# Kernel optimization log

Hardware: AMD Instinct MI355X
Metric: run time of the kernel (lower is better)

## Reference

```python
import jax, jax.numpy as jnp
import numpy as np

TEMPERATURE = 0.1


def setup_inputs() -> dict:
    key = jax.random.key(0)
    k1, k2 = jax.random.split(key)
    B, B_pos, D = 8192, 8192, 1024
    generated = jax.random.normal(k1, (B, D), dtype=jnp.float32)
    positive = jax.random.normal(k2, (B_pos, D), dtype=jnp.float32)
    return {"generated": generated, "positive": positive}


def _pairwise_dist_sq(x, y):
    # (N, M) squared L2 distances, clamped at 0
    x_norm = jnp.sum(x * x, axis=-1, keepdims=True)          # (N, 1)
    y_norm = jnp.sum(y * y, axis=-1, keepdims=True)          # (M, 1)
    d2 = x_norm + y_norm.T - 2.0 * (x @ y.T)
    return jnp.clip(d2, 0.0)


def reference(generated, positive):
    gen = generated.reshape(generated.shape[0], -1)
    pos = positive.reshape(positive.shape[0], -1)
    B = gen.shape[0]

    # Attraction: softmax over distances to positives.
    dist_pos = jnp.sqrt(_pairwise_dist_sq(gen, pos))          # (B, B_pos)
    w_pos = jax.nn.softmax(-dist_pos / TEMPERATURE, axis=1)
    # sum_j w_ij (pos_j - gen_i) == (w_pos @ pos) - gen  (rows of w sum to 1)
    attraction = w_pos @ pos - gen                            # (B, D)

    # Repulsion: softmax over distances to other generated samples (diag masked).
    d2_neg = _pairwise_dist_sq(gen, gen)
    eye = jnp.eye(B, dtype=bool)
    dist_neg = jnp.sqrt(jnp.where(eye, jnp.inf, d2_neg))      # inf diag -> weight 0
    w_neg = jax.nn.softmax(-dist_neg / TEMPERATURE, axis=1)
    repulsion = w_neg @ gen - gen                             # (B, D)

    drift = attraction - repulsion
    target = jax.lax.stop_gradient(gen + drift)
    loss = jnp.mean((gen - target) ** 2)

    drift_norm = jnp.mean(jnp.linalg.norm(drift, axis=-1))
    attraction_norm = jnp.mean(jnp.linalg.norm(attraction, axis=-1))
    repulsion_norm = jnp.mean(jnp.linalg.norm(repulsion, axis=-1))
    return (loss, drift_norm, attraction_norm, repulsion_norm)
```

## Files before the change

kernel.cpp:

```cpp
#include <hip/hip_runtime.h>
#include <stdint.h>

#define INV_T 10.0f
#define SHIFT_ 460.0f
#define MROWS 8192
#define DDIM 1024
#define CHUNK 1024

typedef __attribute__((ext_vector_type(8))) short bf16x8;
typedef __attribute__((ext_vector_type(4))) float f32x4;

__device__ __forceinline__ float bf2f(unsigned short u) {
  return __uint_as_float(((unsigned int)u) << 16);
}
__device__ __forceinline__ unsigned short f2bf(float f) {
  unsigned int u = __float_as_uint(f);
  return (unsigned short)((u + 0x7FFFu + ((u >> 16) & 1u)) >> 16);
}
__device__ __forceinline__ void gl2lds16(const unsigned short* g, unsigned short* l) {
  __builtin_amdgcn_global_load_lds((const __attribute__((address_space(1))) void*)g,
                                   (__attribute__((address_space(3))) void*)l, 16, 0, 0);
}

__global__ void prep_kernel(const float* __restrict__ gen, const float* __restrict__ pos,
                            unsigned short* __restrict__ gen_h, unsigned short* __restrict__ pos_h,
                            float* __restrict__ gn2, float* __restrict__ pn2) {
  int b = blockIdx.x;
  const float* src; unsigned short* dst; float* n2; int row;
  if (b < MROWS) { src = gen; dst = gen_h; n2 = gn2; row = b; }
  else           { src = pos; dst = pos_h; n2 = pn2; row = b - MROWS; }
  int t = threadIdx.x;
  float4 v = ((const float4*)(src + (size_t)row * DDIM))[t];
  float ss = v.x * v.x + v.y * v.y + v.z * v.z + v.w * v.w;
  ushort4 o;
  o.x = f2bf(v.x); o.y = f2bf(v.y); o.z = f2bf(v.z); o.w = f2bf(v.w);
  ((ushort4*)(dst + (size_t)row * DDIM))[t] = o;
#pragma unroll
  for (int m = 1; m < 64; m <<= 1) ss += __shfl_xor(ss, m);
  __shared__ float red[4];
  if ((t & 63) == 0) red[t >> 6] = ss;
  __syncthreads();
  if (t == 0) n2[row] = red[0] + red[1] + red[2] + red[3];
}

__global__ void transpose_kernel(const float* __restrict__ gen, const float* __restrict__ pos,
                                 unsigned short* __restrict__ genT, unsigned short* __restrict__ posT) {
  __shared__ float tile[64][65];
  int b = blockIdx.x;
  const float* src; unsigned short* dst;
  if (b < 2048) { src = gen; dst = genT; }
  else          { src = pos; dst = posT; b -= 2048; }
  int tj = b >> 4, td = b & 15;
  int t = threadIdx.x;
#pragma unroll
  for (int it = 0; it < 16; ++it) {
    int idx = it * 256 + t;
    int r = idx >> 6, c = idx & 63;
    tile[r][c] = src[(size_t)(tj * 64 + r) * DDIM + td * 64 + c];
  }
  __syncthreads();
#pragma unroll
  for (int it = 0; it < 16; ++it) {
    int idx = it * 256 + t;
    int d = idx >> 6, j = idx & 63;
    dst[(size_t)(td * 64 + d) * MROWS + tj * 64 + j] = f2bf(tile[j][d]);
  }
}

template <int EPI>
__launch_bounds__(256, 2)
__global__ void gemm_bt(const unsigned short* __restrict__ A0, const unsigned short* __restrict__ A1,
                        long lda,
                        const unsigned short* __restrict__ B0, const unsigned short* __restrict__ B1,
                        long ldb, int ksteps,
                        unsigned short* __restrict__ P0, unsigned short* __restrict__ P1,
                        int pld, int j0,
                        const float* __restrict__ qn2,
                        const float* __restrict__ kn2a, const float* __restrict__ kn2b,
                        float* __restrict__ lsum0, float* __restrict__ lsum1,
                        unsigned short* __restrict__ O0, unsigned short* __restrict__ O1,
                        int first) {
  __shared__ __align__(16) unsigned short Al[128 * 64];
  __shared__ __align__(16) unsigned short Bl[128 * 64];
  const int z = blockIdx.z;
  const unsigned short* A = z ? A1 : A0;
  const unsigned short* B = z ? B1 : B0;
  const int t = threadIdx.x;
  const int w = t >> 6, lane = t & 63, l15 = lane & 15, quad = lane >> 4;
  const int wm = w >> 1, wn = w & 1;
  const long m0 = (long)blockIdx.x * 128;
  const long n0 = (long)blockIdx.y * 128;
  const int trow = t >> 3;
  const int tcol = (((t & 7) ^ (trow & 7)) * 8);

  f32x4 acc[4][4];
#pragma unroll
  for (int i = 0; i < 4; ++i)
#pragma unroll
    for (int j = 0; j < 4; ++j) acc[i][j] = (f32x4){0.f, 0.f, 0.f, 0.f};

  const unsigned short* Ab = A + (m0 + trow) * lda + tcol;
  const unsigned short* Bb = B + (n0 + trow) * ldb + tcol;
  unsigned short* Alw = Al + t * 8;
  unsigned short* Blw = Bl + t * 8;
  const int ue = (quad ^ (l15 & 7)) * 8;

  for (int ks = 0; ks < ksteps; ++ks) {
    const long ko = (long)ks * 64;
#pragma unroll
    for (int i = 0; i < 4; ++i) gl2lds16(Ab + (long)i * 32 * lda + ko, Alw + i * 2048);
#pragma unroll
    for (int i = 0; i < 4; ++i) gl2lds16(Bb + (long)i * 32 * ldb + ko, Blw + i * 2048);
    __syncthreads();
#pragma unroll
    for (int kk = 0; kk < 2; ++kk) {
      const int uo = ue ^ (kk * 32);
      bf16x8 af[4], bfr[4];
#pragma unroll
      for (int mi = 0; mi < 4; ++mi)
        af[mi] = *(const bf16x8*)(Al + (wm * 64 + mi * 16 + l15) * 64 + uo);
#pragma unroll
      for (int ni = 0; ni < 4; ++ni)
        bfr[ni] = *(const bf16x8*)(Bl + (wn * 64 + ni * 16 + l15) * 64 + uo);
#pragma unroll
      for (int mi = 0; mi < 4; ++mi)
#pragma unroll
        for (int ni = 0; ni < 4; ++ni)
          acc[mi][ni] = __builtin_amdgcn_mfma_f32_16x16x32_bf16(af[mi], bfr[ni], acc[mi][ni], 0, 0, 0);
    }
    __syncthreads();
  }

  if (EPI == 0) {
    unsigned short* Pout = z ? P1 : P0;
    const float* kn2 = z ? kn2b : kn2a;
    float* lsum = z ? lsum1 : lsum0;
#pragma unroll
    for (int mi = 0; mi < 4; ++mi) {
      float rs[4] = {0.f, 0.f, 0.f, 0.f};
#pragma unroll
      for (int ni = 0; ni < 4; ++ni) {
        int c = (int)n0 + wn * 64 + ni * 16 + l15;
        float kn = kn2[j0 + c];
#pragma unroll
        for (int reg = 0; reg < 4; ++reg) {
          long r = m0 + wm * 64 + mi * 16 + quad * 4 + reg;
          float v = acc[mi][ni][reg];
          float d2 = qn2[r] + kn - 2.0f * v;
          float p = __expf(SHIFT_ - INV_T * sqrtf(fmaxf(d2, 0.0f)));
          if (z && (int)r == (j0 + c)) p = 0.0f;
          rs[reg] += p;
          Pout[r * (long)pld + c] = f2bf(p);
        }
      }
#pragma unroll
      for (int reg = 0; reg < 4; ++reg) {
        float v = rs[reg];
        v += __shfl_xor(v, 1); v += __shfl_xor(v, 2);
        v += __shfl_xor(v, 4); v += __shfl_xor(v, 8);
        if (l15 == 0) atomicAdd(&lsum[m0 + wm * 64 + mi * 16 + quad * 4 + reg], v);
      }
    }
  } else {
    unsigned short* Oh = z ? O1 : O0;
#pragma unroll
    for (int mi = 0; mi < 4; ++mi)
#pragma unroll
      for (int ni = 0; ni < 4; ++ni) {
        long c = n0 + wn * 64 + ni * 16 + l15;
#pragma unroll
        for (int reg = 0; reg < 4; ++reg) {
          long r = m0 + wm * 64 + mi * 16 + quad * 4 + reg;
          long off = r * DDIM + c;
          float v = acc[mi][ni][reg];
          Oh[off] = f2bf(first ? v : (bf2f(Oh[off]) + v));
        }
      }
  }
}

__global__ void epi_kernel(const unsigned short* __restrict__ OA, const unsigned short* __restrict__ OR_,
                           const float* __restrict__ lsumA, const float* __restrict__ lsumR,
                           const float* __restrict__ genf, float* __restrict__ gs) {
  __shared__ float wsL[4], wsD[4], wsA[4], wsR[4];
  const int t = threadIdx.x;
  const int w = t >> 6;
  const int lane = t & 63;
  float accL = 0.f, accD = 0.f, accA = 0.f, accR = 0.f;

  for (int i = 0; i < 8; ++i) {
    const int row = blockIdx.x * 32 + w * 8 + i;
    const float invlA = 1.0f / lsumA[row];
    const float invlR = 1.0f / lsumR[row];
    float ssA = 0.f, ssR = 0.f, ssD = 0.f;
#pragma unroll
    for (int u = 0; u < 4; ++u) {
      const long off = (long)row * DDIM + u * 256 + lane * 4;
      float4 g = *(const float4*)(genf + off);
      ushort4 oa = *(const ushort4*)(OA + off);
      ushort4 orr = *(const ushort4*)(OR_ + off);
      float g4[4] = {g.x, g.y, g.z, g.w};
      float a4[4] = {bf2f(oa.x), bf2f(oa.y), bf2f(oa.z), bf2f(oa.w)};
      float r4[4] = {bf2f(orr.x), bf2f(orr.y), bf2f(orr.z), bf2f(orr.w)};
#pragma unroll
      for (int e = 0; e < 4; ++e) {
        float a_ = a4[e] * invlA - g4[e];
        float r_ = r4[e] * invlR - g4[e];
        float d_ = a_ - r_;
        ssA += a_ * a_; ssR += r_ * r_; ssD += d_ * d_;
      }
    }
#pragma unroll
    for (int m = 1; m < 64; m <<= 1) {
      ssA += __shfl_xor(ssA, m);
      ssR += __shfl_xor(ssR, m);
      ssD += __shfl_xor(ssD, m);
    }
    accA += sqrtf(ssA); accR += sqrtf(ssR); accD += sqrtf(ssD); accL += ssD;
  }
  if (lane == 0) { wsL[w] = accL; wsD[w] = accD; wsA[w] = accA; wsR[w] = accR; }
  __syncthreads();
  if (t == 0) {
    atomicAdd(&gs[0], wsL[0] + wsL[1] + wsL[2] + wsL[3]);
    atomicAdd(&gs[1], wsD[0] + wsD[1] + wsD[2] + wsD[3]);
    atomicAdd(&gs[2], wsA[0] + wsA[1] + wsA[2] + wsA[3]);
    atomicAdd(&gs[3], wsR[0] + wsR[1] + wsR[2] + wsR[3]);
  }
}

__global__ void finalize_kernel(const float* __restrict__ gs, float* __restrict__ out) {
  int t = threadIdx.x;
  if (t == 0) out[0] = gs[0] / (8192.0f * 1024.0f);
  if (t == 1) out[1] = gs[1] / 8192.0f;
  if (t == 2) out[2] = gs[2] / 8192.0f;
  if (t == 3) out[3] = gs[3] / 8192.0f;
}

extern "C" void kernel_launch(void* const* d_in, const int* in_sizes, int n_in,
                              void* d_out, int out_size, void* d_ws, size_t ws_size,
                              hipStream_t stream) {
  const float* gen = (const float*)d_in[0];
  const float* pos = (const float*)d_in[1];
  char* ws = (char*)d_ws;
  const size_t MB = (size_t)1 << 20;
  unsigned short* gen_h = (unsigned short*)(ws + 0 * MB);
  unsigned short* pos_h = (unsigned short*)(ws + 16 * MB);
  unsigned short* genT  = (unsigned short*)(ws + 32 * MB);
  unsigned short* posT  = (unsigned short*)(ws + 48 * MB);
  unsigned short* Pa    = (unsigned short*)(ws + 64 * MB);
  unsigned short* Pr    = (unsigned short*)(ws + 80 * MB);
  unsigned short* OhA   = (unsigned short*)(ws + 96 * MB);
  unsigned short* OhR   = (unsigned short*)(ws + 112 * MB);
  float* gn2   = (float*)(ws + 128 * MB);
  float* pn2   = (float*)(ws + 128 * MB + 32768);
  float* lsumA = (float*)(ws + 128 * MB + 65536);
  float* lsumR = (float*)(ws + 128 * MB + 98304);
  float* gs    = (float*)(ws + 128 * MB + 131072);

  hipMemsetAsync(gs, 0, 4 * sizeof(float), stream);
  hipMemsetAsync(lsumA, 0, 2 * MROWS * sizeof(float), stream);
  prep_kernel<<<dim3(16384), dim3(256), 0, stream>>>(gen, pos, gen_h, pos_h, gn2, pn2);
  transpose_kernel<<<dim3(4096), dim3(256), 0, stream>>>(gen, pos, genT, posT);

  const int nchunks = MROWS / CHUNK;
  for (int c = 0; c < nchunks; ++c) {
    const int j0 = c * CHUNK;
    gemm_bt<0><<<dim3(64, CHUNK / 128, 2), dim3(256), 0, stream>>>(
        gen_h, gen_h, DDIM,
        pos_h + (long)j0 * DDIM, gen_h + (long)j0 * DDIM, DDIM, DDIM / 64,
        Pa, Pr, CHUNK, j0, gn2, pn2, gn2, lsumA, lsumR, nullptr, nullptr, 0);
    gemm_bt<1><<<dim3(64, DDIM / 128, 2), dim3(256), 0, stream>>>(
        Pa, Pr, CHUNK,
        posT + j0, genT + j0, MROWS, CHUNK / 64,
        nullptr, nullptr, 0, 0, nullptr, nullptr, nullptr, nullptr, nullptr,
        OhA, OhR, c == 0);
  }

  epi_kernel<<<dim3(256), dim3(256), 0, stream>>>(OhA, OhR, lsumA, lsumR, gen, gs);
  finalize_kernel<<<dim3(1), dim3(64), 0, stream>>>(gs, (float*)d_out);
}
```

Measured before the change: 905.4 us.

## Use 256x256 tiles with 8 waves and a double-buffered pipelined LDS schedule

Measured after the change: 1.021 ms. 1.13x slower.

```diff
diff --git a/kernel.cpp b/kernel.cpp
--- a/kernel.cpp
+++ b/kernel.cpp
@@ -68,7 +68,7 @@
 }
 
 template <int EPI>
-__launch_bounds__(256, 2)
+__launch_bounds__(512, 2)
 __global__ void gemm_bt(const unsigned short* __restrict__ A0, const unsigned short* __restrict__ A1,
                         long lda,
                         const unsigned short* __restrict__ B0, const unsigned short* __restrict__ B1,
@@ -80,63 +80,158 @@
                         float* __restrict__ lsum0, float* __restrict__ lsum1,
                         unsigned short* __restrict__ O0, unsigned short* __restrict__ O1,
                         int first) {
-  __shared__ __align__(16) unsigned short Al[128 * 64];
-  __shared__ __align__(16) unsigned short Bl[128 * 64];
+  __shared__ __align__(16) unsigned short Asm[2][256 * 64];
+  __shared__ __align__(16) unsigned short Bsm[2][256 * 64];
   const int z = blockIdx.z;
   const unsigned short* A = z ? A1 : A0;
   const unsigned short* B = z ? B1 : B0;
   const int t = threadIdx.x;
-  const int w = t >> 6, lane = t & 63, l15 = lane & 15, quad = lane >> 4;
-  const int wm = w >> 1, wn = w & 1;
-  const long m0 = (long)blockIdx.x * 128;
-  const long n0 = (long)blockIdx.y * 128;
+  const int lane = t & 63, l15 = lane & 15, quad = lane >> 4;
+  const int w = t >> 6, wm = w >> 2, wn = w & 3;
+  const long m0 = (long)blockIdx.x * 256;
+  const long n0 = (long)blockIdx.y * 256;
   const int trow = t >> 3;
-  const int tcol = (((t & 7) ^ (trow & 7)) * 8);
-
-  f32x4 acc[4][4];
-#pragma unroll
-  for (int i = 0; i < 4; ++i)
+  const int tcol = ((t & 7) ^ (trow & 7)) * 8;
+  const int uo = (quad ^ (l15 & 7)) * 8;
+
+  const unsigned short* const Ag = A + (m0 + trow) * lda + tcol;
+  const unsigned short* const Bg = B + (n0 + trow) * ldb + tcol;
+
+  f32x4 acc[8][4];
+#pragma unroll
+  for (int i = 0; i < 8; ++i)
 #pragma unroll
     for (int j = 0; j < 4; ++j) acc[i][j] = (f32x4){0.f, 0.f, 0.f, 0.f};
 
-  const unsigned short* Ab = A + (m0 + trow) * lda + tcol;
-  const unsigned short* Bb = B + (n0 + trow) * ldb + tcol;
-  unsigned short* Alw = Al + t * 8;
-  unsigned short* Blw = Bl + t * 8;
-  const int ue = (quad ^ (l15 & 7)) * 8;
+#define ST_A(dst, ko, hf)                                                 \
+  do {                                                                    \
+    const unsigned short* s_ = Ag + (long)((hf) * 128) * lda + (ko);      \
+    unsigned short* d_ = (dst) + (hf) * 8192 + t * 8;                     \
+    gl2lds16(s_, d_);                                                     \
+    gl2lds16(s_ + 64 * lda, d_ + 4096);                                   \
+  } while (0)
+#define ST_B(dst, ko, hf)                                                 \
+  do {                                                                    \
+    const unsigned short* s_ = Bg + (long)((hf) * 128) * ldb + (ko);      \
+    unsigned short* d_ = (dst) + (hf) * 8192 + t * 8;                     \
+    gl2lds16(s_, d_);                                                     \
+    gl2lds16(s_ + 64 * ldb, d_ + 4096);                                   \
+  } while (0)
+
+  ST_A(Asm[0], 0, 0); ST_A(Asm[0], 0, 1);
+  ST_B(Bsm[0], 0, 0); ST_B(Bsm[0], 0, 1);
+  ST_A(Asm[1], 64, 0);
+  asm volatile("s_waitcnt vmcnt(2)" ::: "memory");
+  __builtin_amdgcn_s_barrier();
+
+  unsigned short* Ac = Asm[0]; unsigned short* An = Asm[1];
+  unsigned short* Bc = Bsm[0]; unsigned short* Bn = Bsm[1];
+  const int rbA = (wm * 128 + l15) * 64;
+  const int rbB = (wn * 64 + l15) * 64;
+
+  bf16x8 aR[4][2], bLo[2][2], bHi[2][2];
 
   for (int ks = 0; ks < ksteps; ++ks) {
-    const long ko = (long)ks * 64;
-#pragma unroll
-    for (int i = 0; i < 4; ++i) gl2lds16(Ab + (long)i * 32 * lda + ko, Alw + i * 2048);
-#pragma unroll
-    for (int i = 0; i < 4; ++i) gl2lds16(Bb + (long)i * 32 * ldb + ko, Blw + i * 2048);
-    __syncthreads();
-#pragma unroll
-    for (int kk = 0; kk < 2; ++kk) {
-      const int uo = ue ^ (kk * 32);
-      bf16x8 af[4], bfr[4];
-#pragma unroll
-      for (int mi = 0; mi < 4; ++mi)
-        af[mi] = *(const bf16x8*)(Al + (wm * 64 + mi * 16 + l15) * 64 + uo);
-#pragma unroll
-      for (int ni = 0; ni < 4; ++ni)
-        bfr[ni] = *(const bf16x8*)(Bl + (wn * 64 + ni * 16 + l15) * 64 + uo);
-#pragma unroll
-      for (int mi = 0; mi < 4; ++mi)
-#pragma unroll
-        for (int ni = 0; ni < 4; ++ni)
-          acc[mi][ni] = __builtin_amdgcn_mfma_f32_16x16x32_bf16(af[mi], bfr[ni], acc[mi][ni], 0, 0, 0);
+    const long ko1 = (long)(ks + 1) * 64;
+    const long ko2 = (long)(ks + 2) * 64;
+    const bool s1 = (ks + 1 < ksteps), s2 = (ks + 2 < ksteps);
+
+#pragma unroll
+    for (int mi = 0; mi < 4; ++mi)
+#pragma unroll
+      for (int kk = 0; kk < 2; ++kk)
+        aR[mi][kk] = *(const bf16x8*)(Ac + rbA + mi * 1024 + (uo ^ (kk * 32)));
+#pragma unroll
+    for (int ni = 0; ni < 2; ++ni)
+#pragma unroll
+      for (int kk = 0; kk < 2; ++kk)
+        bLo[ni][kk] = *(const bf16x8*)(Bc + rbB + ni * 1024 + (uo ^ (kk * 32)));
+    if (s1) ST_A(An, ko1, 1);
+    __builtin_amdgcn_s_barrier();
+    asm volatile("s_waitcnt lgkmcnt(0)" ::: "memory");
+    __builtin_amdgcn_sched_barrier(0);
+    __builtin_amdgcn_s_setprio(1);
+#pragma unroll
+    for (int mi = 0; mi < 4; ++mi)
+#pragma unroll
+      for (int ni = 0; ni < 2; ++ni)
+#pragma unroll
+        for (int kk = 0; kk < 2; ++kk)
+          acc[mi][ni] = __builtin_amdgcn_mfma_f32_16x16x32_bf16(aR[mi][kk], bLo[ni][kk], acc[mi][ni], 0, 0, 0);
+    __builtin_amdgcn_s_setprio(0);
+    __builtin_amdgcn_s_barrier();
+
+#pragma unroll
+    for (int ni = 0; ni < 2; ++ni)
+#pragma unroll
+      for (int kk = 0; kk < 2; ++kk)
+        bHi[ni][kk] = *(const bf16x8*)(Bc + rbB + (ni + 2) * 1024 + (uo ^ (kk * 32)));
+    if (s1) ST_B(Bn, ko1, 0);
+    __builtin_amdgcn_s_barrier();
+    asm volatile("s_waitcnt lgkmcnt(0)" ::: "memory");
+    __builtin_amdgcn_sched_barrier(0);
+    __builtin_amdgcn_s_setprio(1);
+#pragma unroll
+    for (int mi = 0; mi < 4; ++mi)
+#pragma unroll
+      for (int ni = 0; ni < 2; ++ni)
+#pragma unroll
+        for (int kk = 0; kk < 2; ++kk)
+          acc[mi][ni + 2] = __builtin_amdgcn_mfma_f32_16x16x32_bf16(aR[mi][kk], bHi[ni][kk], acc[mi][ni + 2], 0, 0, 0);
+    __builtin_amdgcn_s_setprio(0);
+    __builtin_amdgcn_s_barrier();
+
+#pragma unroll
+    for (int mi = 0; mi < 4; ++mi)
+#pragma unroll
+      for (int kk = 0; kk < 2; ++kk)
+        aR[mi][kk] = *(const bf16x8*)(Ac + rbA + (mi + 4) * 1024 + (uo ^ (kk * 32)));
+    if (s1) ST_B(Bn, ko1, 1);
+    __builtin_amdgcn_s_barrier();
+    asm volatile("s_waitcnt lgkmcnt(0)" ::: "memory");
+    __builtin_amdgcn_sched_barrier(0);
+    __builtin_amdgcn_s_setprio(1);
+#pragma unroll
+    for (int mi = 0; mi < 4; ++mi)
+#pragma unroll
+      for (int ni = 0; ni < 2; ++ni)
+#pragma unroll
+        for (int kk = 0; kk < 2; ++kk)
+          acc[mi + 4][ni + 2] = __builtin_amdgcn_mfma_f32_16x16x32_bf16(aR[mi][kk], bHi[ni][kk], acc[mi + 4][ni + 2], 0, 0, 0);
+    __builtin_amdgcn_s_setprio(0);
+    __builtin_amdgcn_s_barrier();
+
+    if (s2) {
+      ST_A(Ac, ko2, 0);
+      asm volatile("s_waitcnt vmcnt(2)" ::: "memory");
+    } else {
+      asm volatile("s_waitcnt vmcnt(0)" ::: "memory");
     }
-    __syncthreads();
-  }
+    __builtin_amdgcn_s_barrier();
+    __builtin_amdgcn_s_setprio(1);
+#pragma unroll
+    for (int mi = 0; mi < 4; ++mi)
+#pragma unroll
+      for (int ni = 0; ni < 2; ++ni)
+#pragma unroll
+        for (int kk = 0; kk < 2; ++kk)
+          acc[mi + 4][ni] = __builtin_amdgcn_mfma_f32_16x16x32_bf16(aR[mi][kk], bLo[ni][kk], acc[mi + 4][ni], 0, 0, 0);
+    __builtin_amdgcn_s_setprio(0);
+    __builtin_amdgcn_s_barrier();
+
+    unsigned short* tp;
+    tp = Ac; Ac = An; An = tp;
+    tp = Bc; Bc = Bn; Bn = tp;
+  }
+#undef ST_A
+#undef ST_B
 
   if (EPI == 0) {
     unsigned short* Pout = z ? P1 : P0;
     const float* kn2 = z ? kn2b : kn2a;
     float* lsum = z ? lsum1 : lsum0;
 #pragma unroll
-    for (int mi = 0; mi < 4; ++mi) {
+    for (int mi = 0; mi < 8; ++mi) {
       float rs[4] = {0.f, 0.f, 0.f, 0.f};
 #pragma unroll
       for (int ni = 0; ni < 4; ++ni) {
@@ -144,7 +239,7 @@
         float kn = kn2[j0 + c];
 #pragma unroll
         for (int reg = 0; reg < 4; ++reg) {
-          long r = m0 + wm * 64 + mi * 16 + quad * 4 + reg;
+          long r = m0 + wm * 128 + mi * 16 + quad * 4 + reg;
           float v = acc[mi][ni][reg];
           float d2 = qn2[r] + kn - 2.0f * v;
           float p = __expf(SHIFT_ - INV_T * sqrtf(fmaxf(d2, 0.0f)));
@@ -158,19 +253,19 @@
         float v = rs[reg];
         v += __shfl_xor(v, 1); v += __shfl_xor(v, 2);
         v += __shfl_xor(v, 4); v += __shfl_xor(v, 8);
-        if (l15 == 0) atomicAdd(&lsum[m0 + wm * 64 + mi * 16 + quad * 4 + reg], v);
+        if (l15 == 0) atomicAdd(&lsum[m0 + wm * 128 + mi * 16 + quad * 4 + reg], v);
       }
     }
   } else {
     unsigned short* Oh = z ? O1 : O0;
 #pragma unroll
-    for (int mi = 0; mi < 4; ++mi)
+    for (int mi = 0; mi < 8; ++mi)
 #pragma unroll
       for (int ni = 0; ni < 4; ++ni) {
         long c = n0 + wn * 64 + ni * 16 + l15;
 #pragma unroll
         for (int reg = 0; reg < 4; ++reg) {
-          long r = m0 + wm * 64 + mi * 16 + quad * 4 + reg;
+          long r = m0 + wm * 128 + mi * 16 + quad * 4 + reg;
           long off = r * DDIM + c;
           float v = acc[mi][ni][reg];
           Oh[off] = f2bf(first ? v : (bf2f(Oh[off]) + v));
@@ -265,11 +360,11 @@
   const int nchunks = MROWS / CHUNK;
   for (int c = 0; c < nchunks; ++c) {
     const int j0 = c * CHUNK;
-    gemm_bt<0><<<dim3(64, CHUNK / 128, 2), dim3(256), 0, stream>>>(
+    gemm_bt<0><<<dim3(MROWS / 256, CHUNK / 256, 2), dim3(512), 0, stream>>>(
         gen_h, gen_h, DDIM,
         pos_h + (long)j0 * DDIM, gen_h + (long)j0 * DDIM, DDIM, DDIM / 64,
         Pa, Pr, CHUNK, j0, gn2, pn2, gn2, lsumA, lsumR, nullptr, nullptr, 0);
-    gemm_bt<1><<<dim3(64, DDIM / 128, 2), dim3(256), 0, stream>>>(
+    gemm_bt<1><<<dim3(MROWS / 256, DDIM / 256, 2), dim3(512), 0, stream>>>(
         Pa, Pr, CHUNK,
         posT + j0, genT + j0, MROWS, CHUNK / 64,
         nullptr, nullptr, 0, 0, nullptr, nullptr, nullptr, nullptr, nullptr,
```

## Share query tile across attraction/repulsion GEMMs and double-chunk the PV GEMM

Applied to the files above, without the earlier changes.

New measurement: 814.2 us. 10.1% less time.

```diff
diff --git a/kernel.cpp b/kernel.cpp
--- a/kernel.cpp
+++ b/kernel.cpp
@@ -67,29 +67,190 @@
   }
 }
 
-template <int EPI>
 __launch_bounds__(256, 2)
-__global__ void gemm_bt(const unsigned short* __restrict__ A0, const unsigned short* __restrict__ A1,
-                        long lda,
-                        const unsigned short* __restrict__ B0, const unsigned short* __restrict__ B1,
-                        long ldb, int ksteps,
-                        unsigned short* __restrict__ P0, unsigned short* __restrict__ P1,
-                        int pld, int j0,
-                        const float* __restrict__ qn2,
-                        const float* __restrict__ kn2a, const float* __restrict__ kn2b,
-                        float* __restrict__ lsum0, float* __restrict__ lsum1,
-                        unsigned short* __restrict__ O0, unsigned short* __restrict__ O1,
+__global__ void gemm_sc(const unsigned short* __restrict__ Aq,
+                        const unsigned short* __restrict__ Bka,
+                        const unsigned short* __restrict__ Bkr,
+                        unsigned short* __restrict__ Pa, unsigned short* __restrict__ Pr,
+                        int j0,
+                        const float* __restrict__ gn2, const float* __restrict__ pn2,
+                        float* __restrict__ lsumA, float* __restrict__ lsumR) {
+  __shared__ __align__(16) unsigned short Al[128 * 64];
+  __shared__ __align__(16) unsigned short Bal[128 * 64];
+  __shared__ __align__(16) unsigned short Brl[128 * 64];
+
+  const int orig = blockIdx.x + 64 * blockIdx.y;
+  const int wid = (orig & 7) * 64 + (orig >> 3);
+  const int by = wid & 7;
+  const int bx = wid >> 3;
+
+  const int t = threadIdx.x;
+  const int w = t >> 6, lane = t & 63, l15 = lane & 15, quad = lane >> 4;
+  const int wm = w >> 1, wn = w & 1;
+  const long m0 = (long)bx * 128;
+  const long n0 = (long)by * 128;
+  const int trow = t >> 3;
+  const int tcol = (((t & 7) ^ (trow & 7)) * 8);
+
+  f32x4 accA[4][4], accR[4][4];
+#pragma unroll
+  for (int i = 0; i < 4; ++i)
+#pragma unroll
+    for (int j = 0; j < 4; ++j) {
+      accA[i][j] = (f32x4){0.f, 0.f, 0.f, 0.f};
+      accR[i][j] = (f32x4){0.f, 0.f, 0.f, 0.f};
+    }
+
+  const unsigned short* Ab  = Aq  + (m0 + trow) * DDIM + tcol;
+  const unsigned short* Bab = Bka + (n0 + trow) * DDIM + tcol;
+  const unsigned short* Brb = Bkr + (n0 + trow) * DDIM + tcol;
+  unsigned short* Alw = Al  + t * 8;
+  unsigned short* Baw = Bal + t * 8;
+  unsigned short* Brw = Brl + t * 8;
+  const int ue = (quad ^ (l15 & 7)) * 8;
+
+  for (int ks = 0; ks < DDIM / 64; ++ks) {
+    const long ko = (long)ks * 64;
+#pragma unroll
+    for (int i = 0; i < 4; ++i) gl2lds16(Ab + (long)i * 32 * DDIM + ko, Alw + i * 2048);
+#pragma unroll
+    for (int i = 0; i < 4; ++i) gl2lds16(Bab + (long)i * 32 * DDIM + ko, Baw + i * 2048);
+#pragma unroll
+    for (int i = 0; i < 4; ++i) gl2lds16(Brb + (long)i * 32 * DDIM + ko, Brw + i * 2048);
+    __syncthreads();
+#pragma unroll
+    for (int kk = 0; kk < 2; ++kk) {
+      const int uo = ue ^ (kk * 32);
+      bf16x8 af[4], ba[4], br[4];
+#pragma unroll
+      for (int mi = 0; mi < 4; ++mi)
+        af[mi] = *(const bf16x8*)(Al + (wm * 64 + mi * 16 + l15) * 64 + uo);
+#pragma unroll
+      for (int ni = 0; ni < 4; ++ni) {
+        ba[ni] = *(const bf16x8*)(Bal + (wn * 64 + ni * 16 + l15) * 64 + uo);
+        br[ni] = *(const bf16x8*)(Brl + (wn * 64 + ni * 16 + l15) * 64 + uo);
+      }
+#pragma unroll
+      for (int mi = 0; mi < 4; ++mi)
+#pragma unroll
+        for (int ni = 0; ni < 4; ++ni) {
+          accA[mi][ni] = __builtin_amdgcn_mfma_f32_16x16x32_bf16(af[mi], ba[ni], accA[mi][ni], 0, 0, 0);
+          accR[mi][ni] = __builtin_amdgcn_mfma_f32_16x16x32_bf16(af[mi], br[ni], accR[mi][ni], 0, 0, 0);
+        }
+    }
+    __syncthreads();
+  }
+
+#pragma unroll
+  for (int mi = 0; mi < 4; ++mi) {
+    float rs[4] = {0.f, 0.f, 0.f, 0.f};
+#pragma unroll
+    for (int ni = 0; ni < 4; ++ni) {
+      int c = (int)n0 + wn * 64 + ni * 16 + l15;
+      float kn = pn2[j0 + c];
+#pragma unroll
+      for (int reg = 0; reg < 4; ++reg) {
+        long r = m0 + wm * 64 + mi * 16 + quad * 4 + reg;
+        float v = accA[mi][ni][reg];
+        float d2 = gn2[r] + kn - 2.0f * v;
+        float p = __expf(SHIFT_ - INV_T * sqrtf(fmaxf(d2, 0.0f)));
+        rs[reg] += p;
+        Pa[r * (long)CHUNK + c] = f2bf(p);
+      }
+    }
+#pragma unroll
+    for (int reg = 0; reg < 4; ++reg) {
+      float v = rs[reg];
+      v += __shfl_xor(v, 1); v += __shfl_xor(v, 2);
+      v += __shfl_xor(v, 4); v += __shfl_xor(v, 8);
+      if (l15 == 0) atomicAdd(&lsumA[m0 + wm * 64 + mi * 16 + quad * 4 + reg], v);
+    }
+  }
+#pragma unroll
+  for (int mi = 0; mi < 4; ++mi) {
+    float rs[4] = {0.f, 0.f, 0.f, 0.f};
+#pragma unroll
+    for (int ni = 0; ni < 4; ++ni) {
+      int c = (int)n0 + wn * 64 + ni * 16 + l15;
+      float kn = gn2[j0 + c];
+#pragma unroll
+      for (int reg = 0; reg < 4; ++reg) {
+        long r = m0 + wm * 64 + mi * 16 + quad * 4 + reg;
+        float v = accR[mi][ni][reg];
+        float d2 = gn2[r] + kn - 2.0f * v;
+        float p = __expf(SHIFT_ - INV_T * sqrtf(fmaxf(d2, 0.0f)));
+        if ((int)r == (j0 + c)) p = 0.0f;
+        rs[reg] += p;
+        Pr[r * (long)CHUNK + c] = f2bf(p);
+      }
+    }
+#pragma unroll
+    for (int reg = 0; reg < 4; ++reg) {
+      float v = rs[reg];
+      v += __shfl_xor(v, 1); v += __shfl_xor(v, 2);
+      v += __shfl_xor(v, 4); v += __shfl_xor(v, 8);
+      if (l15 == 0) atomicAdd(&lsumR[m0 + wm * 64 + mi * 16 + quad * 4 + reg], v);
+    }
+  }
+}
+
+#define KSEG(Abase, Bbase, LDA_, LDB_)                                                     \
+  {                                                                                        \
+    const unsigned short* Ab_ = (Abase) + (m0 + trow) * (LDA_) + tcol;                     \
+    const unsigned short* Bb_ = (Bbase) + (n0 + trow) * (LDB_) + tcol;                     \
+    for (int ks = 0; ks < 16; ++ks) {                                                      \
+      const long ko = (long)ks * 64;                                                       \
+      _Pragma("unroll")                                                                    \
+      for (int i = 0; i < 4; ++i) gl2lds16(Ab_ + (long)i * 32 * (LDA_) + ko, Alw + i * 2048); \
+      _Pragma("unroll")                                                                    \
+      for (int i = 0; i < 4; ++i) gl2lds16(Bb_ + (long)i * 32 * (LDB_) + ko, Blw + i * 2048); \
+      __syncthreads();                                                                     \
+      _Pragma("unroll")                                                                    \
+      for (int kk = 0; kk < 2; ++kk) {                                                     \
+        const int uo = ue ^ (kk * 32);                                                     \
+        bf16x8 af[4], bfr[4];                                                              \
+        _Pragma("unroll")                                                                  \
+        for (int mi = 0; mi < 4; ++mi)                                                     \
+          af[mi] = *(const bf16x8*)(Al + (wm * 64 + mi * 16 + l15) * 64 + uo);             \
+        _Pragma("unroll")                                                                  \
+        for (int ni = 0; ni < 4; ++ni)                                                     \
+          bfr[ni] = *(const bf16x8*)(Bl + (wn * 64 + ni * 16 + l15) * 64 + uo);            \
+        _Pragma("unroll")                                                                  \
+        for (int mi = 0; mi < 4; ++mi)                                                     \
+          _Pragma("unroll")                                                                \
+          for (int ni = 0; ni < 4; ++ni)                                                   \
+            acc[mi][ni] = __builtin_amdgcn_mfma_f32_16x16x32_bf16(af[mi], bfr[ni], acc[mi][ni], 0, 0, 0); \
+      }                                                                                    \
+      __syncthreads();                                                                     \
+    }                                                                                      \
+  }
+
+__launch_bounds__(256, 2)
+__global__ void gemm_pv(const unsigned short* __restrict__ Pa0, const unsigned short* __restrict__ Pr0,
+                        const unsigned short* __restrict__ Pa1, const unsigned short* __restrict__ Pr1,
+                        const unsigned short* __restrict__ Va0, const unsigned short* __restrict__ Vr0,
+                        const unsigned short* __restrict__ Va1, const unsigned short* __restrict__ Vr1,
+                        unsigned short* __restrict__ OA, unsigned short* __restrict__ OR_,
                         int first) {
   __shared__ __align__(16) unsigned short Al[128 * 64];
   __shared__ __align__(16) unsigned short Bl[128 * 64];
-  const int z = blockIdx.z;
-  const unsigned short* A = z ? A1 : A0;
-  const unsigned short* B = z ? B1 : B0;
+
+  const int orig = blockIdx.x + 64 * (blockIdx.y + 8 * blockIdx.z);
+  const int wid = (orig & 7) * 128 + (orig >> 3);
+  const int by = wid & 7;
+  const int bx = (wid >> 3) & 63;
+  const int z = wid >> 9;
+
+  const unsigned short* A0 = z ? Pr0 : Pa0;
+  const unsigned short* B0 = z ? Vr0 : Va0;
+  const unsigned short* A1 = z ? Pr1 : Pa1;
+  const unsigned short* B1 = z ? Vr1 : Va1;
+
   const int t = threadIdx.x;
   const int w = t >> 6, lane = t & 63, l15 = lane & 15, quad = lane >> 4;
   const int wm = w >> 1, wn = w & 1;
-  const long m0 = (long)blockIdx.x * 128;
-  const long n0 = (long)blockIdx.y * 128;
+  const long m0 = (long)bx * 128;
+  const long n0 = (long)by * 128;
   const int trow = t >> 3;
   const int tcol = (((t & 7) ^ (trow & 7)) * 8);
 
@@ -99,85 +260,29 @@
 #pragma unroll
     for (int j = 0; j < 4; ++j) acc[i][j] = (f32x4){0.f, 0.f, 0.f, 0.f};
 
-  const unsigned short* Ab = A + (m0 + trow) * lda + tcol;
-  const unsigned short* Bb = B + (n0 + trow) * ldb + tcol;
   unsigned short* Alw = Al + t * 8;
   unsigned short* Blw = Bl + t * 8;
   const int ue = (quad ^ (l15 & 7)) * 8;
 
-  for (int ks = 0; ks < ksteps; ++ks) {
-    const long ko = (long)ks * 64;
-#pragma unroll
-    for (int i = 0; i < 4; ++i) gl2lds16(Ab + (long)i * 32 * lda + ko, Alw + i * 2048);
-#pragma unroll
-    for (int i = 0; i < 4; ++i) gl2lds16(Bb + (long)i * 32 * ldb + ko, Blw + i * 2048);
-    __syncthreads();
-#pragma unroll
-    for (int kk = 0; kk < 2; ++kk) {
-      const int uo = ue ^ (kk * 32);
-      bf16x8 af[4], bfr[4];
-#pragma unroll
-      for (int mi = 0; mi < 4; ++mi)
-        af[mi] = *(const bf16x8*)(Al + (wm * 64 + mi * 16 + l15) * 64 + uo);
-#pragma unroll
-      for (int ni = 0; ni < 4; ++ni)
-        bfr[ni] = *(const bf16x8*)(Bl + (wn * 64 + ni * 16 + l15) * 64 + uo);
-#pragma unroll
-      for (int mi = 0; mi < 4; ++mi)
-#pragma unroll
-        for (int ni = 0; ni < 4; ++ni)
-          acc[mi][ni] = __builtin_amdgcn_mfma_f32_16x16x32_bf16(af[mi], bfr[ni], acc[mi][ni], 0, 0, 0);
-    }
-    __syncthreads();
-  }
-
-  if (EPI == 0) {
-    unsigned short* Pout = z ? P1 : P0;
-    const float* kn2 = z ? kn2b : kn2a;
-    float* lsum = z ? lsum1 : lsum0;
-#pragma unroll
-    for (int mi = 0; mi < 4; ++mi) {
-      float rs[4] = {0.f, 0.f, 0.f, 0.f};
-#pragma unroll
-      for (int ni = 0; ni < 4; ++ni) {
-        int c = (int)n0 + wn * 64 + ni * 16 + l15;
-        float kn = kn2[j0 + c];
-#pragma unroll
-        for (int reg = 0; reg < 4; ++reg) {
-          long r = m0 + wm * 64 + mi * 16 + quad * 4 + reg;
-          float v = acc[mi][ni][reg];
-          float d2 = qn2[r] + kn - 2.0f * v;
-          float p = __expf(SHIFT_ - INV_T * sqrtf(fmaxf(d2, 0.0f)));
-          if (z && (int)r == (j0 + c)) p = 0.0f;
-          rs[reg] += p;
-          Pout[r * (long)pld + c] = f2bf(p);
-        }
-      }
+  KSEG(A0, B0, CHUNK, MROWS);
+  KSEG(A1, B1, CHUNK, MROWS);
+
+  unsigned short* Oh = z ? OR_ : OA;
+#pragma unroll
+  for (int mi = 0; mi < 4; ++mi)
+#pragma unroll
+    for (int ni = 0; ni < 4; ++ni) {
+      long c = n0 + wn * 64 + ni * 16 + l15;
 #pragma unroll
       for (int reg = 0; reg < 4; ++reg) {
-        float v = rs[reg];
-        v += __shfl_xor(v, 1); v += __shfl_xor(v, 2);
-        v += __shfl_xor(v, 4); v += __shfl_xor(v, 8);
-        if (l15 == 0) atomicAdd(&lsum[m0 + wm * 64 + mi * 16 + quad * 4 + reg], v);
-      }
-    }
-  } else {
-    unsigned short* Oh = z ? O1 : O0;
-#pragma unroll
-    for (int mi = 0; mi < 4; ++mi)
-#pragma unroll
-      for (int ni = 0; ni < 4; ++ni) {
-        long c = n0 + wn * 64 + ni * 16 + l15;
-#pragma unroll
-        for (int reg = 0; reg < 4; ++reg) {
-          long r = m0 + wm * 64 + mi * 16 + quad * 4 + reg;
-          long off = r * DDIM + c;
-          float v = acc[mi][ni][reg];
-          Oh[off] = f2bf(first ? v : (bf2f(Oh[off]) + v));
-        }
-      }
-  }
-}
+        long r = m0 + wm * 64 + mi * 16 + quad * 4 + reg;
+        long off = r * DDIM + c;
+        float v = acc[mi][ni][reg];
+        Oh[off] = f2bf(first ? v : (bf2f(Oh[off]) + v));
+      }
+    }
+}
+#undef KSEG
 
 __global__ void epi_kernel(const unsigned short* __restrict__ OA, const unsigned short* __restrict__ OR_,
                            const float* __restrict__ lsumA, const float* __restrict__ lsumR,
@@ -247,33 +352,35 @@
   unsigned short* pos_h = (unsigned short*)(ws + 16 * MB);
   unsigned short* genT  = (unsigned short*)(ws + 32 * MB);
   unsigned short* posT  = (unsigned short*)(ws + 48 * MB);
-  unsigned short* Pa    = (unsigned short*)(ws + 64 * MB);
-  unsigned short* Pr    = (unsigned short*)(ws + 80 * MB);
-  unsigned short* OhA   = (unsigned short*)(ws + 96 * MB);
-  unsigned short* OhR   = (unsigned short*)(ws + 112 * MB);
-  float* gn2   = (float*)(ws + 128 * MB);
-  float* pn2   = (float*)(ws + 128 * MB + 32768);
-  float* lsumA = (float*)(ws + 128 * MB + 65536);
-  float* lsumR = (float*)(ws + 128 * MB + 98304);
-  float* gs    = (float*)(ws + 128 * MB + 131072);
+  unsigned short* Pa0   = (unsigned short*)(ws + 64 * MB);
+  unsigned short* Pr0   = (unsigned short*)(ws + 80 * MB);
+  unsigned short* Pa1   = (unsigned short*)(ws + 96 * MB);
+  unsigned short* Pr1   = (unsigned short*)(ws + 112 * MB);
+  unsigned short* OhA   = (unsigned short*)(ws + 128 * MB);
+  unsigned short* OhR   = (unsigned short*)(ws + 144 * MB);
+  float* gn2   = (float*)(ws + 160 * MB);
+  float* pn2   = (float*)(ws + 160 * MB + 32768);
+  float* lsumA = (float*)(ws + 160 * MB + 65536);
+  float* lsumR = (float*)(ws + 160 * MB + 98304);
+  float* gs    = (float*)(ws + 160 * MB + 131072);
 
   hipMemsetAsync(gs, 0, 4 * sizeof(float), stream);
   hipMemsetAsync(lsumA, 0, 2 * MROWS * sizeof(float), stream);
   prep_kernel<<<dim3(16384), dim3(256), 0, stream>>>(gen, pos, gen_h, pos_h, gn2, pn2);
   transpose_kernel<<<dim3(4096), dim3(256), 0, stream>>>(gen, pos, genT, posT);
 
-  const int nchunks = MROWS / CHUNK;
-  for (int c = 0; c < nchunks; ++c) {
-    const int j0 = c * CHUNK;
-    gemm_bt<0><<<dim3(64, CHUNK / 128, 2), dim3(256), 0, stream>>>(
-        gen_h, gen_h, DDIM,
-        pos_h + (long)j0 * DDIM, gen_h + (long)j0 * DDIM, DDIM, DDIM / 64,
-        Pa, Pr, CHUNK, j0, gn2, pn2, gn2, lsumA, lsumR, nullptr, nullptr, 0);
-    gemm_bt<1><<<dim3(64, DDIM / 128, 2), dim3(256), 0, stream>>>(
-        Pa, Pr, CHUNK,
-        posT + j0, genT + j0, MROWS, CHUNK / 64,
-        nullptr, nullptr, 0, 0, nullptr, nullptr, nullptr, nullptr, nullptr,
-        OhA, OhR, c == 0);
+  for (int p = 0; p < 4; ++p) {
+    const int j00 = (2 * p) * CHUNK, j01 = (2 * p + 1) * CHUNK;
+    gemm_sc<<<dim3(64, 8), dim3(256), 0, stream>>>(
+        gen_h, pos_h + (long)j00 * DDIM, gen_h + (long)j00 * DDIM,
+        Pa0, Pr0, j00, gn2, pn2, lsumA, lsumR);
+    gemm_sc<<<dim3(64, 8), dim3(256), 0, stream>>>(
+        gen_h, pos_h + (long)j01 * DDIM, gen_h + (long)j01 * DDIM,
+        Pa1, Pr1, j01, gn2, pn2, lsumA, lsumR);
+    gemm_pv<<<dim3(64, 8, 2), dim3(256), 0, stream>>>(
+        Pa0, Pr0, Pa1, Pr1,
+        posT + j00, genT + j00, posT + j01, genT + j01,
+        OhA, OhR, p == 0);
   }
 
   epi_kernel<<<dim3(256), dim3(256), 0, stream>>>(OhA, OhR, lsumA, lsumR, gen, gs);
```
